# Optimization experiments

Measured on AMD Instinct MI355X. Metric: run time of the kernel, lower is better.

Reference implementation:

```python
import jax, jax.numpy as jnp
import numpy as np

C_IN = 512
C = 64        # per-head dim
N_HEAD = 8
B, S = 2, 2048


def setup_inputs() -> dict:
    key = jax.random.key(0)
    ks = jax.random.split(key, 9)
    scale = 1.0 / np.sqrt(C_IN)
    return {
        "x": jax.random.normal(ks[0], (B, S, C_IN), dtype=jnp.float32),
        "bias": jax.random.normal(ks[1], (B, N_HEAD, S, S), dtype=jnp.float32),
        "Wq": jax.random.normal(ks[2], (N_HEAD * C, C_IN), dtype=jnp.float32) * scale,
        "Wk": jax.random.normal(ks[3], (N_HEAD * C, C_IN), dtype=jnp.float32) * scale,
        "Wv": jax.random.normal(ks[4], (N_HEAD * C, C_IN), dtype=jnp.float32) * scale,
        "Wo": jax.random.normal(ks[5], (C_IN, N_HEAD * C), dtype=jnp.float32) * scale,
        "bo": jax.random.normal(ks[6], (C_IN,), dtype=jnp.float32) * 0.01,
        "Wg": jax.random.normal(ks[7], (N_HEAD * C, C_IN), dtype=jnp.float32) * scale,
        "bg": jax.random.normal(ks[8], (N_HEAD * C,), dtype=jnp.float32) * 0.01,
    }


def reference(x, bias, Wq, Wk, Wv, Wo, bo, Wg, bg):
    # x: [B, S, C_IN]; attn_dim=1 -> q/k/v axis is already at -2 after movedim.
    # Project and split heads: [B, S, H*C] -> [B, H, S, C]
    def split_heads(t):
        Bq, Sq, _ = t.shape
        return t.reshape(Bq, Sq, N_HEAD, C).transpose(0, 2, 1, 3)

    q = split_heads(x @ Wq.T) / jnp.sqrt(jnp.asarray(C, x.dtype))
    k = split_heads(x @ Wk.T)
    v = split_heads(x @ Wv.T)

    a = jnp.einsum("bhqc,bhkc->bhqk", q, k) + bias   # [B, H, S, S]
    a = jax.nn.softmax(a, axis=-1)
    o = jnp.einsum("bhqk,bhkc->bhqc", a, v)          # [B, H, S, C]

    # merge heads back: [B, S, H*C]
    o = o.transpose(0, 2, 1, 3).reshape(x.shape[0], x.shape[1], N_HEAD * C)
    g = jax.nn.sigmoid(x @ Wg.T + bg)
    o = g * o
    return o @ Wo.T + bo                              # [B, S, C_IN]
```

## Files before the change

### kernel.cpp

```cpp
#include <hip/hip_runtime.h>
#include <math.h>

#define BB 2
#define HH 8
#define SS 2048
#define CC 64
#define CIN 512
#define DDIM 512
#define MM (BB*SS)
#define KSPLIT 2
#define KDOM (SS / KSPLIT)
#define NCHUNK (KDOM / 64)

#define LOG2E 1.4426950408889634f
#define SHIFT2 (16.0f * LOG2E)

using short8  = __attribute__((ext_vector_type(8))) short;
using float4v = __attribute__((ext_vector_type(4))) float;

__device__ __forceinline__ unsigned short tob(float f) {
    unsigned u = __float_as_uint(f);
    unsigned r = (u + 0x7fffu + ((u >> 16) & 1u)) >> 16;
    return (unsigned short)r;
}
__device__ __forceinline__ float fromb(unsigned short u) {
    return __uint_as_float(((unsigned)u) << 16);
}

__device__ __forceinline__ void barrier_lds_only() {
    __builtin_amdgcn_sched_barrier(0);
    asm volatile("s_waitcnt lgkmcnt(0)" ::: "memory");
    __builtin_amdgcn_s_barrier();
    __builtin_amdgcn_sched_barrier(0);
}

__global__ __launch_bounds__(256) void convert_all(
    const float* __restrict__ x,
    const float* __restrict__ wq, const float* __restrict__ wk,
    const float* __restrict__ wv, const float* __restrict__ wg,
    const float* __restrict__ wo,
    unsigned short* __restrict__ xb,
    unsigned short* __restrict__ wqb, unsigned short* __restrict__ wkb,
    unsigned short* __restrict__ wvb, unsigned short* __restrict__ wgb,
    unsigned short* __restrict__ wob)
{
    const int NX4 = MM * CIN / 4;
    int i = blockIdx.x * blockDim.x + threadIdx.x;
    const float* src; unsigned short* dst; float scale = 1.0f; int off;
    if (i < NX4) { src = x; dst = xb; off = i; }
    else {
        int j = i - NX4;
        int seg = j >> 16;
        off = j & 65535;
        if      (seg == 0) { src = wq; dst = wqb; scale = 0.125f * LOG2E; }
        else if (seg == 1) { src = wk; dst = wkb; }
        else if (seg == 2) { src = wv; dst = wvb; }
        else if (seg == 3) { src = wg; dst = wgb; }
        else               { src = wo; dst = wob; }
    }
    float4 v = ((const float4*)src)[off];
    ushort4 o;
    o.x = tob(v.x * scale); o.y = tob(v.y * scale);
    o.z = tob(v.z * scale); o.w = tob(v.w * scale);
    ((ushort4*)dst)[off] = o;
}

__global__ __launch_bounds__(256) void proj_gemm(
    const unsigned short* __restrict__ X,
    const unsigned short* __restrict__ Wq,
    const unsigned short* __restrict__ Wk,
    const unsigned short* __restrict__ Wv,
    const unsigned short* __restrict__ Wg,
    const float* __restrict__ bg,
    unsigned short* __restrict__ Qd,
    unsigned short* __restrict__ Kd,
    unsigned short* __restrict__ Vd,
    unsigned short* __restrict__ Gd)
{
    __shared__ __align__(16) unsigned short At[64][72];
    __shared__ __align__(16) unsigned short Bt[64][72];

    int mode = blockIdx.z;
    const unsigned short* W = (mode == 0) ? Wq : (mode == 1) ? Wk : (mode == 2) ? Wv : Wg;

    int m0 = blockIdx.y * 64;
    int n0 = blockIdx.x * 64;
    int tid = threadIdx.x;
    int w = tid >> 6, lane = tid & 63;
    int quad = lane >> 4, l16 = lane & 15;
    int wm = w & 1, wn = w >> 1;

    float4v acc[2][2];
    for (int a = 0; a < 2; ++a) for (int c = 0; c < 2; ++c) acc[a][c] = (float4v)0.0f;

    for (int kc = 0; kc < CIN; kc += 64) {
        for (int it = 0; it < 2; ++it) {
            int idx = it * 2048 + tid * 8;
            int row = idx >> 6, col = idx & 63;
            *(short8*)&At[row][col] = *(const short8*)&X[(size_t)(m0 + row) * CIN + kc + col];
            *(short8*)&Bt[row][col] = *(const short8*)&W[(size_t)(n0 + row) * CIN + kc + col];
        }
        __syncthreads();
        for (int ks = 0; ks < 2; ++ks) {
            short8 a0 = *(const short8*)&At[wm * 32 + l16][ks * 32 + quad * 8];
            short8 a1 = *(const short8*)&At[wm * 32 + 16 + l16][ks * 32 + quad * 8];
            short8 b0 = *(const short8*)&Bt[wn * 32 + l16][ks * 32 + quad * 8];
            short8 b1 = *(const short8*)&Bt[wn * 32 + 16 + l16][ks * 32 + quad * 8];
            acc[0][0] = __builtin_amdgcn_mfma_f32_16x16x32_bf16(a0, b0, acc[0][0], 0, 0, 0);
            acc[0][1] = __builtin_amdgcn_mfma_f32_16x16x32_bf16(a0, b1, acc[0][1], 0, 0, 0);
            acc[1][0] = __builtin_amdgcn_mfma_f32_16x16x32_bf16(a1, b0, acc[1][0], 0, 0, 0);
            acc[1][1] = __builtin_amdgcn_mfma_f32_16x16x32_bf16(a1, b1, acc[1][1], 0, 0, 0);
        }
        __syncthreads();
    }

    if (mode == 2) {
        for (int a = 0; a < 2; ++a) for (int c = 0; c < 2; ++c)
            for (int r = 0; r < 4; ++r) {
                int ml = wm * 32 + a * 16 + quad * 4 + r;
                int nl = wn * 32 + c * 16 + l16;
                At[nl][ml] = tob(acc[a][c][r]);
            }
        __syncthreads();
        int bi = m0 >> 11, h = n0 >> 6, s0 = m0 & 2047;
        int crow = tid >> 2, seg = tid & 3;
        unsigned short* dp = Vd + (((size_t)(bi * HH + h) * CC) + crow) * SS + s0 + seg * 16;
        *(short8*)dp       = *(const short8*)&At[crow][seg * 16];
        *(short8*)(dp + 8) = *(const short8*)&At[crow][seg * 16 + 8];
        return;
    }

    for (int a = 0; a < 2; ++a) for (int c = 0; c < 2; ++c)
        for (int r = 0; r < 4; ++r) {
            int gm = m0 + wm * 32 + a * 16 + quad * 4 + r;
            int gn = n0 + wn * 32 + c * 16 + l16;
            float v = acc[a][c][r];
            if (mode <= 1) {
                int bi = gm >> 11, s = gm & 2047, h = gn >> 6, cc = gn & 63;
                unsigned short* d = (mode == 0) ? Qd : Kd;
                d[(((size_t)(bi * HH + h) * SS) + s) * CC + cc] = tob(v);
            } else {
                float g = 1.0f / (1.0f + __expf(-(v + bg[gn])));
                Gd[(size_t)gm * DDIM + gn] = tob(g);
            }
        }
}

__global__ __launch_bounds__(256) void attn_kernel(
    const unsigned short* __restrict__ Q,
    const unsigned short* __restrict__ K,
    const unsigned short* __restrict__ V,
    const float* __restrict__ bias,
    float* __restrict__ part,
    float* __restrict__ Ls)
{
    __shared__ __align__(16) unsigned short Kt[64][72];
    __shared__ __align__(16) unsigned short Vt[64][72];
    __shared__ __align__(16) unsigned short Pt[4][16][72];

    int qb = blockIdx.x * 64;
    int bh = blockIdx.y;
    int split = blockIdx.z;
    int ksbase = split * KDOM;
    int b = bh >> 3, h = bh & 7;
    int tid = threadIdx.x;
    int w = tid >> 6, lane = tid & 63;
    int quad = lane >> 4, l16 = lane & 15;

    int phase = (blockIdx.x + blockIdx.y + 8 * blockIdx.z) & (NCHUNK - 1);

    const unsigned short* Qbh = Q + (size_t)bh * SS * CC;
    const unsigned short* Kbh = K + (size_t)bh * SS * CC + (size_t)ksbase * CC;
    const unsigned short* Vbh = V + (size_t)bh * CC * SS + ksbase;
    const float* brow0 = bias + (size_t)bh * SS * SS
                       + (size_t)(qb + w * 16 + quad * 4) * SS + ksbase + l16;

    int qrow = qb + w * 16 + l16;
    short8 aq0 = *(const short8*)&Qbh[(size_t)qrow * CC + quad * 8];
    short8 aq1 = *(const short8*)&Qbh[(size_t)qrow * CC + 32 + quad * 8];

    float lsum[4] = {0.f, 0.f, 0.f, 0.f};
    float4v accO[4];
    for (int jn = 0; jn < 4; ++jn) accO[jn] = (float4v)0.0f;

    int srow0 = (tid * 8) >> 6,        scol0 = (tid * 8) & 63;
    int srow1 = (2048 + tid * 8) >> 6, scol1 = (2048 + tid * 8) & 63;

    short8 pk[2][2], pv[2][2];
    float  bb[2][4][4];
    {
        int kb0 = phase * 64;
        pk[0][0] = *(const short8*)&Kbh[(size_t)(kb0 + srow0) * CC + scol0];
        pk[0][1] = *(const short8*)&Kbh[(size_t)(kb0 + srow1) * CC + scol1];
        pv[0][0] = *(const short8*)&Vbh[(size_t)srow0 * SS + kb0 + scol0];
        pv[0][1] = *(const short8*)&Vbh[(size_t)srow1 * SS + kb0 + scol1];
#pragma unroll
        for (int j = 0; j < 4; ++j)
#pragma unroll
            for (int r = 0; r < 4; ++r)
                bb[0][j][r] = brow0[r * SS + kb0 + j * 16];
    }

#pragma unroll
    for (int c = 0; c < NCHUNK; ++c) {
        barrier_lds_only();
        *(short8*)&Kt[srow0][scol0] = pk[c & 1][0];
        *(short8*)&Kt[srow1][scol1] = pk[c & 1][1];
        *(short8*)&Vt[srow0][scol0] = pv[c & 1][0];
        *(short8*)&Vt[srow1][scol1] = pv[c & 1][1];

        if (c + 1 < NCHUNK) {
            int kbn = ((c + 1 + phase) & (NCHUNK - 1)) * 64;
            pk[(c + 1) & 1][0] = *(const short8*)&Kbh[(size_t)(kbn + srow0) * CC + scol0];
            pk[(c + 1) & 1][1] = *(const short8*)&Kbh[(size_t)(kbn + srow1) * CC + scol1];
            pv[(c + 1) & 1][0] = *(const short8*)&Vbh[(size_t)srow0 * SS + kbn + scol0];
            pv[(c + 1) & 1][1] = *(const short8*)&Vbh[(size_t)srow1 * SS + kbn + scol1];
#pragma unroll
            for (int j = 0; j < 4; ++j)
#pragma unroll
                for (int r = 0; r < 4; ++r)
                    bb[(c + 1) & 1][j][r] = brow0[r * SS + kbn + j * 16];
        }

        barrier_lds_only();

        float4v sa[4];
#pragma unroll
        for (int j = 0; j < 4; ++j) sa[j] = (float4v)(-SHIFT2);
#pragma unroll
        for (int j = 0; j < 4; ++j) {
            short8 bk0 = *(const short8*)&Kt[j * 16 + l16][quad * 8];
            short8 bk1 = *(const short8*)&Kt[j * 16 + l16][32 + quad * 8];
            sa[j] = __builtin_amdgcn_mfma_f32_16x16x32_bf16(aq0, bk0, sa[j], 0, 0, 0);
            sa[j] = __builtin_amdgcn_mfma_f32_16x16x32_bf16(aq1, bk1, sa[j], 0, 0, 0);
        }

#pragma unroll
        for (int j = 0; j < 4; ++j)
#pragma unroll
            for (int r = 0; r < 4; ++r) {
                float p = __builtin_amdgcn_exp2f(fmaf(bb[c & 1][j][r], LOG2E, sa[j][r]));
                lsum[r] += p;
                Pt[w][quad * 4 + r][j * 16 + l16] = tob(p);
            }

#pragma unroll
        for (int ks = 0; ks < 2; ++ks) {
            short8 ap = *(const short8*)&Pt[w][l16][ks * 32 + quad * 8];
#pragma unroll
            for (int jn = 0; jn < 4; ++jn) {
                short8 bv = *(const short8*)&Vt[jn * 16 + l16][ks * 32 + quad * 8];
                accO[jn] = __builtin_amdgcn_mfma_f32_16x16x32_bf16(ap, bv, accO[jn], 0, 0, 0);
            }
        }
    }

    for (int r = 0; r < 4; ++r) {
        float s = lsum[r];
        s += __shfl_xor(s, 1, 64);
        s += __shfl_xor(s, 2, 64);
        s += __shfl_xor(s, 4, 64);
        s += __shfl_xor(s, 8, 64);
        lsum[r] = s;
    }

    int mrow = b * SS + qb + w * 16 + quad * 4;
    float* pOut = part + (size_t)split * MM * DDIM;
    for (int jn = 0; jn < 4; ++jn)
        for (int r = 0; r < 4; ++r)
            pOut[(size_t)(mrow + r) * DDIM + h * 64 + jn * 16 + l16] = accO[jn][r];
    if (l16 == 0)
        for (int r = 0; r < 4; ++r)
            Ls[((size_t)split * MM + mrow + r) * HH + h] = lsum[r];
}

__global__ __launch_bounds__(256) void combine_kernel(
    const float* __restrict__ part,
    const float* __restrict__ Ls,
    const unsigned short* __restrict__ G,
    unsigned short* __restrict__ Og)
{
    int i = blockIdx.x * 256 + threadIdx.x;
    int row = i >> 7;
    int c4  = (i & 127) << 2;
    int h   = c4 >> 6;
    float l = 0.f;
#pragma unroll
    for (int s = 0; s < KSPLIT; ++s)
        l += Ls[((size_t)s * MM + row) * HH + h];
    float rl = 1.0f / l;
    float ax = 0.f, ay = 0.f, az = 0.f, aw = 0.f;
#pragma unroll
    for (int s = 0; s < KSPLIT; ++s) {
        float4 t = *(const float4*)(part + (size_t)s * MM * DDIM + (size_t)row * DDIM + c4);
        ax += t.x; ay += t.y; az += t.z; aw += t.w;
    }
    ushort4 g = *(const ushort4*)&G[(size_t)row * DDIM + c4];
    ushort4 o;
    o.x = tob(ax * rl * fromb(g.x));
    o.y = tob(ay * rl * fromb(g.y));
    o.z = tob(az * rl * fromb(g.z));
    o.w = tob(aw * rl * fromb(g.w));
    *(ushort4*)&Og[(size_t)row * DDIM + c4] = o;
}

__global__ __launch_bounds__(256) void out_gemm(
    const unsigned short* __restrict__ Og,
    const unsigned short* __restrict__ W,
    const float* __restrict__ bo,
    float* __restrict__ out)
{
    __shared__ __align__(16) unsigned short At[64][72];
    __shared__ __align__(16) unsigned short Bt[64][72];

    int m0 = blockIdx.y * 64;
    int n0 = blockIdx.x * 64;
    int tid = threadIdx.x;
    int w = tid >> 6, lane = tid & 63;
    int quad = lane >> 4, l16 = lane & 15;
    int wm = w & 1, wn = w >> 1;

    float4v acc[2][2];
    for (int a = 0; a < 2; ++a) for (int c = 0; c < 2; ++c) acc[a][c] = (float4v)0.0f;

    for (int kc = 0; kc < DDIM; kc += 64) {
        for (int it = 0; it < 2; ++it) {
            int idx = it * 2048 + tid * 8;
            int row = idx >> 6, col = idx & 63;
            *(short8*)&At[row][col] = *(const short8*)&Og[(size_t)(m0 + row) * DDIM + kc + col];
            *(short8*)&Bt[row][col] = *(const short8*)&W[(size_t)(n0 + row) * DDIM + kc + col];
        }
        __syncthreads();
        for (int ks = 0; ks < 2; ++ks) {
            short8 a0 = *(const short8*)&At[wm * 32 + l16][ks * 32 + quad * 8];
            short8 a1 = *(const short8*)&At[wm * 32 + 16 + l16][ks * 32 + quad * 8];
            short8 b0 = *(const short8*)&Bt[wn * 32 + l16][ks * 32 + quad * 8];
            short8 b1 = *(const short8*)&Bt[wn * 32 + 16 + l16][ks * 32 + quad * 8];
            acc[0][0] = __builtin_amdgcn_mfma_f32_16x16x32_bf16(a0, b0, acc[0][0], 0, 0, 0);
            acc[0][1] = __builtin_amdgcn_mfma_f32_16x16x32_bf16(a0, b1, acc[0][1], 0, 0, 0);
            acc[1][0] = __builtin_amdgcn_mfma_f32_16x16x32_bf16(a1, b0, acc[1][0], 0, 0, 0);
            acc[1][1] = __builtin_amdgcn_mfma_f32_16x16x32_bf16(a1, b1, acc[1][1], 0, 0, 0);
        }
        __syncthreads();
    }

    for (int a = 0; a < 2; ++a) for (int c = 0; c < 2; ++c)
        for (int r = 0; r < 4; ++r) {
            int gm = m0 + wm * 32 + a * 16 + quad * 4 + r;
            int gn = n0 + wn * 32 + c * 16 + l16;
            out[(size_t)gm * DDIM + gn] = acc[a][c][r] + bo[gn];
        }
}

extern "C" void kernel_launch(void* const* d_in, const int* in_sizes, int n_in,
                              void* d_out, int out_size, void* d_ws, size_t ws_size,
                              hipStream_t stream)
{
    const float* x    = (const float*)d_in[0];
    const float* bias = (const float*)d_in[1];
    const float* Wq   = (const float*)d_in[2];
    const float* Wk   = (const float*)d_in[3];
    const float* Wv   = (const float*)d_in[4];
    const float* Wo   = (const float*)d_in[5];
    const float* bo   = (const float*)d_in[6];
    const float* Wg   = (const float*)d_in[7];
    const float* bg   = (const float*)d_in[8];
    float* out = (float*)d_out;

    char* ws = (char*)d_ws;
    auto alloc = [&](size_t bytes) { char* p = ws; ws += (bytes + 255) & ~(size_t)255; return p; };
    unsigned short* xb  = (unsigned short*)alloc((size_t)MM * CIN * 2);
    unsigned short* wqb = (unsigned short*)alloc((size_t)DDIM * CIN * 2);
    unsigned short* wkb = (unsigned short*)alloc((size_t)DDIM * CIN * 2);
    unsigned short* wvb = (unsigned short*)alloc((size_t)DDIM * CIN * 2);
    unsigned short* wgb = (unsigned short*)alloc((size_t)DDIM * CIN * 2);
    unsigned short* wob = (unsigned short*)alloc((size_t)DDIM * CIN * 2);
    unsigned short* Qh  = (unsigned short*)alloc((size_t)BB * HH * SS * CC * 2);
    unsigned short* Kh  = (unsigned short*)alloc((size_t)BB * HH * SS * CC * 2);
    unsigned short* Vh  = (unsigned short*)alloc((size_t)BB * HH * SS * CC * 2);
    unsigned short* Gt  = (unsigned short*)alloc((size_t)MM * DDIM * 2);
    unsigned short* Om  = (unsigned short*)alloc((size_t)MM * DDIM * 2);
    float* part = (float*)alloc((size_t)KSPLIT * MM * DDIM * 4);
    float* Lsum = (float*)alloc((size_t)KSPLIT * MM * HH * 4);

    convert_all<<<3328, 256, 0, stream>>>(x, Wq, Wk, Wv, Wg, Wo,
                                          xb, wqb, wkb, wvb, wgb, wob);
    proj_gemm<<<dim3(DDIM / 64, MM / 64, 4), 256, 0, stream>>>(
        xb, wqb, wkb, wvb, wgb, bg, Qh, Kh, Vh, Gt);
    attn_kernel<<<dim3(SS / 64, BB * HH, KSPLIT), 256, 0, stream>>>(
        Qh, Kh, Vh, bias, part, Lsum);
    combine_kernel<<<(MM * DDIM / 4) / 256, 256, 0, stream>>>(part, Lsum, Gt, Om);
    out_gemm<<<dim3(DDIM / 64, MM / 64), 256, 0, stream>>>(Om, wob, bo, out);
}
```

Before: 436.5 us.

## Drop key split, fuse combine into attention, stage bias through LDS

Result: slower. 493.0 us (+12.9%).

```diff
diff --git a/kernel.cpp b/kernel.cpp
--- a/kernel.cpp
+++ b/kernel.cpp
@@ -8,9 +8,7 @@
 #define CIN 512
 #define DDIM 512
 #define MM (BB*SS)
-#define KSPLIT 2
-#define KDOM (SS / KSPLIT)
-#define NCHUNK (KDOM / 64)
+#define NCHUNK (SS / 64)
 
 #define LOG2E 1.4426950408889634f
 #define SHIFT2 (16.0f * LOG2E)
@@ -146,34 +144,32 @@
         }
 }
 
-__global__ __launch_bounds__(256) void attn_kernel(
+__global__ __launch_bounds__(256, 2) void attn_kernel(
     const unsigned short* __restrict__ Q,
     const unsigned short* __restrict__ K,
     const unsigned short* __restrict__ V,
     const float* __restrict__ bias,
-    float* __restrict__ part,
-    float* __restrict__ Ls)
+    const unsigned short* __restrict__ G,
+    unsigned short* __restrict__ Om)
 {
     __shared__ __align__(16) unsigned short Kt[64][72];
     __shared__ __align__(16) unsigned short Vt[64][72];
     __shared__ __align__(16) unsigned short Pt[4][16][72];
+    __shared__ __align__(16) float Bs[64][68];
 
     int qb = blockIdx.x * 64;
     int bh = blockIdx.y;
-    int split = blockIdx.z;
-    int ksbase = split * KDOM;
     int b = bh >> 3, h = bh & 7;
     int tid = threadIdx.x;
     int w = tid >> 6, lane = tid & 63;
     int quad = lane >> 4, l16 = lane & 15;
 
-    int phase = (blockIdx.x + blockIdx.y + 8 * blockIdx.z) & (NCHUNK - 1);
+    int phase = (blockIdx.x + blockIdx.y) & (NCHUNK - 1);
 
     const unsigned short* Qbh = Q + (size_t)bh * SS * CC;
-    const unsigned short* Kbh = K + (size_t)bh * SS * CC + (size_t)ksbase * CC;
-    const unsigned short* Vbh = V + (size_t)bh * CC * SS + ksbase;
-    const float* brow0 = bias + (size_t)bh * SS * SS
-                       + (size_t)(qb + w * 16 + quad * 4) * SS + ksbase + l16;
+    const unsigned short* Kbh = K + (size_t)bh * SS * CC;
+    const unsigned short* Vbh = V + (size_t)bh * CC * SS;
+    const float* Bbh = bias + (size_t)bh * SS * SS;
 
     int qrow = qb + w * 16 + l16;
     short8 aq0 = *(const short8*)&Qbh[(size_t)qrow * CC + quad * 8];
@@ -185,41 +181,41 @@
 
     int srow0 = (tid * 8) >> 6,        scol0 = (tid * 8) & 63;
     int srow1 = (2048 + tid * 8) >> 6, scol1 = (2048 + tid * 8) & 63;
-
-    short8 pk[2][2], pv[2][2];
-    float  bb[2][4][4];
+    int btrow = tid >> 4;
+    int btcol = (tid & 15) * 4;
+
+    short8 pk0, pk1, pv0, pv1;
+    float4 pb[4];
     {
         int kb0 = phase * 64;
-        pk[0][0] = *(const short8*)&Kbh[(size_t)(kb0 + srow0) * CC + scol0];
-        pk[0][1] = *(const short8*)&Kbh[(size_t)(kb0 + srow1) * CC + scol1];
-        pv[0][0] = *(const short8*)&Vbh[(size_t)srow0 * SS + kb0 + scol0];
-        pv[0][1] = *(const short8*)&Vbh[(size_t)srow1 * SS + kb0 + scol1];
-#pragma unroll
-        for (int j = 0; j < 4; ++j)
-#pragma unroll
-            for (int r = 0; r < 4; ++r)
-                bb[0][j][r] = brow0[r * SS + kb0 + j * 16];
-    }
-
-#pragma unroll
+        pk0 = *(const short8*)&Kbh[(size_t)(kb0 + srow0) * CC + scol0];
+        pk1 = *(const short8*)&Kbh[(size_t)(kb0 + srow1) * CC + scol1];
+        pv0 = *(const short8*)&Vbh[(size_t)srow0 * SS + kb0 + scol0];
+        pv1 = *(const short8*)&Vbh[(size_t)srow1 * SS + kb0 + scol1];
+#pragma unroll
+        for (int rr = 0; rr < 4; ++rr)
+            pb[rr] = *(const float4*)&Bbh[(size_t)(qb + rr * 16 + btrow) * SS + kb0 + btcol];
+    }
+
     for (int c = 0; c < NCHUNK; ++c) {
         barrier_lds_only();
-        *(short8*)&Kt[srow0][scol0] = pk[c & 1][0];
-        *(short8*)&Kt[srow1][scol1] = pk[c & 1][1];
-        *(short8*)&Vt[srow0][scol0] = pv[c & 1][0];
-        *(short8*)&Vt[srow1][scol1] = pv[c & 1][1];
+        *(short8*)&Kt[srow0][scol0] = pk0;
+        *(short8*)&Kt[srow1][scol1] = pk1;
+        *(short8*)&Vt[srow0][scol0] = pv0;
+        *(short8*)&Vt[srow1][scol1] = pv1;
+#pragma unroll
+        for (int rr = 0; rr < 4; ++rr)
+            *(float4*)&Bs[rr * 16 + btrow][btcol] = pb[rr];
 
         if (c + 1 < NCHUNK) {
             int kbn = ((c + 1 + phase) & (NCHUNK - 1)) * 64;
-            pk[(c + 1) & 1][0] = *(const short8*)&Kbh[(size_t)(kbn + srow0) * CC + scol0];
-            pk[(c + 1) & 1][1] = *(const short8*)&Kbh[(size_t)(kbn + srow1) * CC + scol1];
-            pv[(c + 1) & 1][0] = *(const short8*)&Vbh[(size_t)srow0 * SS + kbn + scol0];
-            pv[(c + 1) & 1][1] = *(const short8*)&Vbh[(size_t)srow1 * SS + kbn + scol1];
-#pragma unroll
-            for (int j = 0; j < 4; ++j)
-#pragma unroll
-                for (int r = 0; r < 4; ++r)
-                    bb[(c + 1) & 1][j][r] = brow0[r * SS + kbn + j * 16];
+            pk0 = *(const short8*)&Kbh[(size_t)(kbn + srow0) * CC + scol0];
+            pk1 = *(const short8*)&Kbh[(size_t)(kbn + srow1) * CC + scol1];
+            pv0 = *(const short8*)&Vbh[(size_t)srow0 * SS + kbn + scol0];
+            pv1 = *(const short8*)&Vbh[(size_t)srow1 * SS + kbn + scol1];
+#pragma unroll
+            for (int rr = 0; rr < 4; ++rr)
+                pb[rr] = *(const float4*)&Bbh[(size_t)(qb + rr * 16 + btrow) * SS + kbn + btcol];
         }
 
         barrier_lds_only();
@@ -239,7 +235,8 @@
         for (int j = 0; j < 4; ++j)
 #pragma unroll
             for (int r = 0; r < 4; ++r) {
-                float p = __builtin_amdgcn_exp2f(fmaf(bb[c & 1][j][r], LOG2E, sa[j][r]));
+                float bb = Bs[w * 16 + quad * 4 + r][j * 16 + l16];
+                float p = __builtin_amdgcn_exp2f(fmaf(bb, LOG2E, sa[j][r]));
                 lsum[r] += p;
                 Pt[w][quad * 4 + r][j * 16 + l16] = tob(p);
             }
@@ -255,53 +252,26 @@
         }
     }
 
+    float rl[4];
+#pragma unroll
     for (int r = 0; r < 4; ++r) {
         float s = lsum[r];
         s += __shfl_xor(s, 1, 64);
         s += __shfl_xor(s, 2, 64);
         s += __shfl_xor(s, 4, 64);
         s += __shfl_xor(s, 8, 64);
-        lsum[r] = s;
+        rl[r] = 1.0f / s;
     }
 
     int mrow = b * SS + qb + w * 16 + quad * 4;
-    float* pOut = part + (size_t)split * MM * DDIM;
+#pragma unroll
     for (int jn = 0; jn < 4; ++jn)
-        for (int r = 0; r < 4; ++r)
-            pOut[(size_t)(mrow + r) * DDIM + h * 64 + jn * 16 + l16] = accO[jn][r];
-    if (l16 == 0)
-        for (int r = 0; r < 4; ++r)
-            Ls[((size_t)split * MM + mrow + r) * HH + h] = lsum[r];
-}
-
-__global__ __launch_bounds__(256) void combine_kernel(
-    const float* __restrict__ part,
-    const float* __restrict__ Ls,
-    const unsigned short* __restrict__ G,
-    unsigned short* __restrict__ Og)
-{
-    int i = blockIdx.x * 256 + threadIdx.x;
-    int row = i >> 7;
-    int c4  = (i & 127) << 2;
-    int h   = c4 >> 6;
-    float l = 0.f;
-#pragma unroll
-    for (int s = 0; s < KSPLIT; ++s)
-        l += Ls[((size_t)s * MM + row) * HH + h];
-    float rl = 1.0f / l;
-    float ax = 0.f, ay = 0.f, az = 0.f, aw = 0.f;
-#pragma unroll
-    for (int s = 0; s < KSPLIT; ++s) {
-        float4 t = *(const float4*)(part + (size_t)s * MM * DDIM + (size_t)row * DDIM + c4);
-        ax += t.x; ay += t.y; az += t.z; aw += t.w;
-    }
-    ushort4 g = *(const ushort4*)&G[(size_t)row * DDIM + c4];
-    ushort4 o;
-    o.x = tob(ax * rl * fromb(g.x));
-    o.y = tob(ay * rl * fromb(g.y));
-    o.z = tob(az * rl * fromb(g.z));
-    o.w = tob(aw * rl * fromb(g.w));
-    *(ushort4*)&Og[(size_t)row * DDIM + c4] = o;
+#pragma unroll
+        for (int r = 0; r < 4; ++r) {
+            int col = h * 64 + jn * 16 + l16;
+            float g = fromb(G[(size_t)(mrow + r) * DDIM + col]);
+            Om[(size_t)(mrow + r) * DDIM + col] = tob(accO[jn][r] * rl[r] * g);
+        }
 }
 
 __global__ __launch_bounds__(256) void out_gemm(
@@ -380,15 +350,12 @@
     unsigned short* Vh  = (unsigned short*)alloc((size_t)BB * HH * SS * CC * 2);
     unsigned short* Gt  = (unsigned short*)alloc((size_t)MM * DDIM * 2);
     unsigned short* Om  = (unsigned short*)alloc((size_t)MM * DDIM * 2);
-    float* part = (float*)alloc((size_t)KSPLIT * MM * DDIM * 4);
-    float* Lsum = (float*)alloc((size_t)KSPLIT * MM * HH * 4);
 
     convert_all<<<3328, 256, 0, stream>>>(x, Wq, Wk, Wv, Wg, Wo,
                                           xb, wqb, wkb, wvb, wgb, wob);
     proj_gemm<<<dim3(DDIM / 64, MM / 64, 4), 256, 0, stream>>>(
         xb, wqb, wkb, wvb, wgb, bg, Qh, Kh, Vh, Gt);
-    attn_kernel<<<dim3(SS / 64, BB * HH, KSPLIT), 256, 0, stream>>>(
-        Qh, Kh, Vh, bias, part, Lsum);
-    combine_kernel<<<(MM * DDIM / 4) / 256, 256, 0, stream>>>(part, Lsum, Gt, Om);
+    attn_kernel<<<dim3(SS / 64, BB * HH), 256, 0, stream>>>(
+        Qh, Kh, Vh, bias, Gt, Om);
     out_gemm<<<dim3(DDIM / 64, MM / 64), 256, 0, stream>>>(Om, wob, bo, out);
 }
```
